# Kernel tuning notes

Measured on AMD Instinct MI355X. Metric: run time of the kernel, lower is better.

Reference implementation:

```python
import jax, jax.numpy as jnp
import numpy as np

N = 50000      # amino-acid nodes
DIN = 64       # input feature dim
DH = 64        # hidden dim (= GAT out_feats per head)
H = 4          # attention heads
E_RES, E_SEQ, E_KNN = 400000, 100000, 400000
EPS = 1e-5


def setup_inputs() -> dict:
    key = jax.random.key(0)
    ks = iter(jax.random.split(key, 32))
    def nrm(shape, scale=0.1):
        return jax.random.normal(next(ks), shape, dtype=jnp.float32) * scale
    def edges(E):
        s = jax.random.randint(next(ks), (E,), 0, N, dtype=jnp.int32)
        d = jax.random.randint(next(ks), (E,), 0, N, dtype=jnp.int32)
        return s, d
    x = nrm((N, DIN), 1.0)
    src_res, dst_res = edges(E_RES)
    src_seq, dst_seq = edges(E_SEQ)
    src_knn, dst_knn = edges(E_KNN)
    inp = dict(x=x, src_res=src_res, dst_res=dst_res, src_seq=src_seq,
               dst_seq=dst_seq, src_knn=src_knn, dst_knn=dst_knn)
    # layer 0 (in=DIN), layer 1 (in=DH): per-relation stacked GAT params
    inp.update(W0=nrm((3, DIN, H * DH)), al0=nrm((3, H, DH)), ar0=nrm((3, H, DH)),
               b0=nrm((3, H * DH)), rW0=nrm((3, DIN, H * DH)))
    inp.update(W1=nrm((3, DH, H * DH)), al1=nrm((3, H, DH)), ar1=nrm((3, H, DH)),
               b1=nrm((3, H * DH)), rW1=nrm((3, DH, H * DH)))
    inp.update(fcW0=nrm((DH, DH)), fcb0=nrm((DH,)), fcW1=nrm((DH, DH)), fcb1=nrm((DH,)))
    inp.update(g0=jnp.ones((DIN,), jnp.float32), be0=jnp.zeros((DIN,), jnp.float32),
               g1=jnp.ones((DH,), jnp.float32), be1=jnp.zeros((DH,), jnp.float32))
    return inp


def _bn(x, g, b):
    mu = jnp.mean(x, axis=0)
    var = jnp.mean((x - mu) ** 2, axis=0)
    return (x - mu) * jax.lax.rsqrt(var + EPS) * g + b


def _gat(h, src, dst, W, al, ar, bias, rW):
    # DGL GATConv (feat_drop off in eval, residual=True via res_fc Linear, bias)
    n = h.shape[0]
    fs = (h @ W).reshape(n, H, DH)                    # [N,H,D]
    el = jnp.sum(fs * al, axis=-1)                    # [N,H]
    er = jnp.sum(fs * ar, axis=-1)
    e = jax.nn.leaky_relu(el[src] + er[dst], 0.2)     # [E,H]
    m = jax.ops.segment_max(e, dst, num_segments=n)
    a = jnp.exp(e - m[dst])
    s = jax.ops.segment_sum(a, dst, num_segments=n)
    alpha = a / s[dst]                                # edge-softmax per dst/head
    rst = jax.ops.segment_sum(alpha[:, :, None] * fs[src], dst, num_segments=n)
    return rst + (h @ rW).reshape(n, H, DH) + bias.reshape(1, H, DH)


def _layer(x, edges, W, al, ar, b, rW, fcW, fcb, g, be):
    x = _bn(x, g, be)
    h = jnp.zeros((x.shape[0], H, DH), x.dtype)
    for r, (s_, d_) in enumerate(edges):              # 3 relation types, summed
        h = h + _gat(x, s_, d_, W[r], al[r], ar[r], b[r], rW[r])
    x = jnp.mean(h, axis=1)                           # mean over heads
    return jax.nn.relu(x @ fcW + fcb)


def reference(x, src_res, dst_res, src_seq, dst_seq, src_knn, dst_knn,
              W0, al0, ar0, b0, rW0, W1, al1, ar1, b1, rW1,
              fcW0, fcb0, fcW1, fcb1, g0, be0, g1, be1):
    edges = [(src_res, dst_res), (src_seq, dst_seq), (src_knn, dst_knn)]
    x = _layer(x, edges, W0, al0, ar0, b0, rW0, fcW0, fcb0, g0, be0)
    x = _layer(x, edges, W1, al1, ar1, b1, rW1, fcW1, fcb1, g1, be1)
    return x
```

## Files before the change

### kernel.cpp

```cpp
#include <hip/hip_runtime.h>
#include <math.h>

#define NN    50000
#define DD    64
#define HH    4
#define E_RES 400000
#define E_SEQ 100000
#define E_KNN 400000
#define ETOT  (E_RES+E_SEQ+E_KNN)
#define RPS   (NN + 4)
#define MBLK  ((NN+63)/64)
#define NBLK  ((NN+255)/256)
#define ZS    800
#define KTOT  864
#define CTPS  (ETOT + 32)
#define NGRP  (NN/4)
#define AGB   ((3*NGRP)/4)
#define NBUK  98
#define TBUK  (3*NBUK)
#define EPB   4096
#define PABLK ((ETOT+EPB-1)/EPB)

typedef __attribute__((ext_vector_type(8))) short short8;
typedef __attribute__((ext_vector_type(4))) float floatx4;

__device__ inline unsigned short f2bf(float f){
  union{float f; unsigned u;} v; v.f=f;
  unsigned r = v.u + 0x7FFF + ((v.u>>16)&1);
  return (unsigned short)(r>>16);
}
__device__ inline float bf2f(unsigned short u){
  union{unsigned u; float f;} v; v.u=(unsigned)u<<16; return v.f;
}


__global__ void __launch_bounds__(256)
k_bucketcnt(const int* __restrict__ d0, const int* __restrict__ d1,
            const int* __restrict__ d2, int* __restrict__ bcnt){
  __shared__ int cnt[TBUK];
  int t = threadIdx.x;
  for(int i=t;i<TBUK;i+=256) cnt[i]=0;
  __syncthreads();
  int ebase = blockIdx.x*EPB;
  #pragma unroll
  for(int j=0;j<16;j++){
    int i = ebase + j*256 + t;
    int d, r;
    if(i < E_RES){ d=d0[i]; r=0; }
    else if(i < E_RES+E_SEQ){ d=d1[i-E_RES]; r=1; }
    else if(i < ETOT){ d=d2[i-E_RES-E_SEQ]; r=2; }
    else continue;
    atomicAdd(&cnt[r*NBUK + (d>>9)], 1);
  }
  __syncthreads();
  for(int i=t;i<TBUK;i+=256){ int c=cnt[i]; if(c) atomicAdd(&bcnt[i], c); }
}

__global__ void k_bucketscan(const int* __restrict__ bcnt,
                             int* __restrict__ bbase, int* __restrict__ bcur){
  __shared__ int sh[TBUK];
  int t = threadIdx.x;
  if(t < 64){
    int carry = 0;
    for(int c=0;c<5;c++){
      int idx = c*64 + t;
      int v = (idx < TBUK) ? bcnt[idx] : 0;
      int inc = v;
      for(int off=1; off<64; off<<=1){ int n=__shfl_up(inc, off, 64); if(t>=off) inc+=n; }
      if(idx < TBUK) sh[idx] = carry + inc - v;
      carry += __shfl(inc, 63, 64);
    }
  }
  __syncthreads();
  if(t < TBUK){ bbase[t] = sh[t]; bcur[t] = sh[t]; }
  if(t == 0) bbase[TBUK] = ETOT;
}

__global__ void __launch_bounds__(256)
k_partA(const int* __restrict__ s0, const int* __restrict__ d0,
        const int* __restrict__ s1, const int* __restrict__ d1,
        const int* __restrict__ s2, const int* __restrict__ d2,
        int* __restrict__ bcur, unsigned* __restrict__ pairs){
  __shared__ int cnt[TBUK];
  __shared__ int gb[TBUK];
  int t = threadIdx.x;
  for(int i=t;i<TBUK;i+=256) cnt[i]=0;
  __syncthreads();
  int ebase = blockIdx.x*EPB;
  unsigned meta[16], pk[16];
  #pragma unroll
  for(int j=0;j<16;j++){
    int i = ebase + j*256 + t;
    int s, d, r;
    if(i < E_RES){ s=s0[i]; d=d0[i]; r=0; }
    else if(i < E_RES+E_SEQ){ int k=i-E_RES; s=s1[k]; d=d1[k]; r=1; }
    else if(i < ETOT){ int k=i-E_RES-E_SEQ; s=s2[k]; d=d2[k]; r=2; }
    else { meta[j]=0xFFFFFFFFu; continue; }
    int bk = r*NBUK + (d>>9);
    int rk = atomicAdd(&cnt[bk], 1);
    meta[j] = ((unsigned)bk<<16) | (unsigned)rk;
    pk[j]   = ((unsigned)(d&511)<<16) | (unsigned)s;
  }
  __syncthreads();
  for(int i=t;i<TBUK;i+=256){ int c=cnt[i]; gb[i] = c ? atomicAdd(&bcur[i], c) : 0; }
  __syncthreads();
  #pragma unroll
  for(int j=0;j<16;j++){
    unsigned mt = meta[j];
    if(mt != 0xFFFFFFFFu)
      pairs[gb[mt>>16] + (mt & 0xFFFFu)] = pk[j];
  }
}

__global__ void __launch_bounds__(256)
k_partB(const unsigned* __restrict__ pairs, const int* __restrict__ bbase,
        int* __restrict__ rowptr, int* __restrict__ csr){
  int bb = blockIdx.x, r = bb / NBUK, b = bb - r*NBUK;
  int dbase = b*512, dmax = min(512, NN - dbase);
  int off = (r==0)?0:(r==1)?E_RES:(E_RES+E_SEQ);
  __shared__ int hist[512];
  __shared__ int curs[513];
  int t = threadIdx.x;
  hist[t]=0; hist[256+t]=0;
  __syncthreads();
  int beg = bbase[bb], end = bbase[bb+1];
  for(int i=beg+t; i<end; i+=256) atomicAdd(&hist[pairs[i]>>16], 1);
  __syncthreads();
  if(t < 64){
    int carry = 0;
    for(int c=0;c<8;c++){
      int v = hist[c*64+t];
      int inc = v;
      for(int o2=1; o2<64; o2<<=1){ int n=__shfl_up(inc, o2, 64); if(t>=o2) inc+=n; }
      curs[c*64+t] = (beg - off) + carry + inc - v;
      carry += __shfl(inc, 63, 64);
    }
    if(t==0) curs[512] = end - off;
  }
  __syncthreads();
  int* rp = rowptr + r*RPS + dbase;
  for(int i=t; i<=dmax; i+=256) rp[i] = curs[i];
  __syncthreads();
  for(int i=beg+t; i<end; i+=256){
    unsigned p = pairs[i];
    int pos = atomicAdd(&curs[p>>16], 1);
    csr[off + pos] = (int)(p & 0xFFFFu);
  }
}

__global__ void k_bnstats(const float* __restrict__ x, float* __restrict__ stats,
                          unsigned short* __restrict__ Abf){
  __shared__ float sh[512];
  int t = threadIdx.x, col = t & 63, rg = t >> 6;
  float s=0.f, q=0.f;
  for(int row = blockIdx.x*4 + rg; row < NN; row += gridDim.x*4){
    float v = x[(size_t)row*64 + col]; s += v; q += v*v;
    Abf[(size_t)row*64 + col] = f2bf(v);
  }
  sh[t]=s; sh[256+t]=q; __syncthreads();
  if(rg==0){
    s = sh[col]+sh[64+col]+sh[128+col]+sh[192+col];
    q = sh[256+col]+sh[320+col]+sh[384+col]+sh[448+col];
    atomicAdd(&stats[col], s); atomicAdd(&stats[64+col], q);
  }
}

__global__ void __launch_bounds__(256)
k_prep3(const float* __restrict__ stats, const float* __restrict__ g,
        const float* __restrict__ be, const float* __restrict__ W,
        const float* __restrict__ al, const float* __restrict__ ar,
        const float* __restrict__ b, const float* __restrict__ rW,
        const float* __restrict__ fcW, const float* __restrict__ fcb,
        float* __restrict__ wbufF){
  __shared__ float scale[64], shift[64];
  int t = threadIdx.x;
  if(t<64){
    float mu  = stats[t]*(1.0f/NN);
    float var = stats[64+t]*(1.0f/NN) - mu*mu;
    float sc  = g[t]*rsqrtf(var + 1e-5f);
    scale[t]=sc; shift[t]=be[t]-mu*sc;
  }
  __syncthreads();
  char* wb = (char*)wbufF;
  unsigned short* Wf = (unsigned short*)wbufF;
  float* biasF = (float*)(wb + 110592);
  int bid = blockIdx.x;
  if(bid < 52){
    __shared__ float fcWs[4096];
    for(int i=t;i<4096;i+=256) fcWs[i]=fcW[i];
    __syncthreads();
    int j = bid*16 + (t>>4);
    int cg = (t&15)*4;
    float Wrow[64];
    if(j < 64){
      for(int d=0; d<64; d++){
        float w=0.f;
        for(int r=0;r<3;r++)
          #pragma unroll
          for(int h=0;h<4;h++)
            w += rW[((size_t)(r*64+j))*256 + h*64 + d];
        Wrow[d] = scale[j]*0.25f*w;
      }
    } else {
      int jj = j-64;
      int r = jj>>8, dc = jj&255, h = dc&3, c = dc>>2;
      const float* Wp = W + ((size_t)(r*64+c))*256 + h*64;
      float sc = 0.25f*scale[c];
      #pragma unroll
      for(int d=0; d<64; d++) Wrow[d] = sc*Wp[d];
    }
    #pragma unroll
    for(int cc=0; cc<4; cc++){
      int col = cg+cc;
      float acc=0.f;
      #pragma unroll
      for(int d=0; d<64; d++) acc += Wrow[d]*fcWs[d*64+col];
      Wf[(size_t)col*KTOT + j] = f2bf(acc);
    }
  } else if(bid < 58){
    int wv = (bid-52)*4 + (t>>6);
    int r = wv >> 3, cc = wv & 7, h = cc & 3, k = t & 63;
    const float* av = ((cc>=4)?ar:al) + (r*HH+h)*64;
    const float* Wk = W + ((size_t)(r*64+k))*256 + h*64;
    float w=0.f;
    for(int d2=0; d2<64; d2++) w += Wk[d2]*av[d2];
    float* WelR = (float*)(wb + 110848 + r*2080);
    WelR[cc*64 + k] = scale[k]*w;
    float bp = shift[k]*w;
    for(int off=32; off; off>>=1) bp += __shfl_down(bp, off, 64);
    if(k==0) (WelR + 512)[cc] = bp;
  } else {
    __shared__ float S[3][64];
    __shared__ float BH[64];
    if(t<192){
      int r=t>>6, d=t&63;
      float s=0.f;
      #pragma unroll
      for(int h=0;h<4;h++){
        const float* Wp = W + (size_t)(r*64)*256 + h*64 + d;
        for(int k=0;k<64;k++) s += shift[k]*Wp[(size_t)k*256];
      }
      S[r][d]=0.25f*s;
    } else {
      int d = t-192;
      float s=0.f;
      for(int k=0;k<64;k++){
        float w=0.f;
        for(int r=0;r<3;r++)
          #pragma unroll
          for(int h=0;h<4;h++)
            w += rW[((size_t)(r*64+k))*256 + h*64 + d];
        s += shift[k]*0.25f*w;
      }
      float bb=0.f;
      for(int r=0;r<3;r++)
        #pragma unroll
        for(int h=0;h<4;h++) bb += b[r*256 + h*64 + d];
      BH[d] = s + 0.25f*bb;
    }
    __syncthreads();
    if(t<192){
      int r=t>>6, col=t&63;
      float acc=0.f;
      for(int d=0;d<64;d++) acc += S[r][d]*fcW[d*64+col];
      Wf[(size_t)col*KTOT + 832 + r] = f2bf(acc);
    } else {
      int col=t-192;
      float acc=0.f;
      for(int d=0;d<64;d++) acc += BH[d]*fcW[d*64+col];
      biasF[col] = acc + fcb[col];
    }
    if(t<64){
      for(int j=835;j<KTOT;j++) Wf[(size_t)t*KTOT + j] = 0;
    }
  }
}

__global__ void __launch_bounds__(256)
k_el3(const float* __restrict__ A, const float* __restrict__ wbufF,
      float* __restrict__ EL){
  int r = blockIdx.x / NBLK;
  const char* wb = (const char*)wbufF;
  const float* Wel = (const float*)(wb + 110848 + r*2080);
  const float* biasE = Wel + 512;
  float* ELr = EL + (size_t)r*NN*8;
  __shared__ float sw[512];
  __shared__ float sb[8];
  int t = threadIdx.x;
  sw[t]=Wel[t]; sw[256+t]=Wel[256+t];
  if(t<8) sb[t]=biasE[t];
  __syncthreads();
  int n = (blockIdx.x % NBLK)*256 + t;
  if(n>=NN) return;
  float acc[8];
  #pragma unroll
  for(int c=0;c<8;c++) acc[c]=sb[c];
  const float4* Ar = (const float4*)(A + (size_t)n*64);
  #pragma unroll
  for(int kq=0;kq<16;kq++){
    float4 a = Ar[kq];
    #pragma unroll
    for(int c=0;c<8;c++){
      const float* w = sw + c*64 + kq*4;
      acc[c] += a.x*w[0] + a.y*w[1] + a.z*w[2] + a.w*w[3];
    }
  }
  ((float4*)ELr)[n*2]   = make_float4(acc[0],acc[1],acc[2],acc[3]);
  ((float4*)ELr)[n*2+1] = make_float4(acc[4],acc[5],acc[6],acc[7]);
}

__global__ void __launch_bounds__(256)
k_edgecoef3(const float* __restrict__ EL, const int* __restrict__ rowptr,
            const int* __restrict__ csr, unsigned short* __restrict__ coefT){
  int r = blockIdx.x / NBLK;
  const float* ELr = EL + (size_t)r*NN*8;
  const int* rp = rowptr + r*RPS;
  int off = (r==0)?0:(r==1)?E_RES:(E_RES+E_SEQ);
  const int* cs = csr + off;
  unsigned short* t0 = coefT + off;
  unsigned short* t1 = coefT + (size_t)CTPS + off;
  unsigned short* t2 = coefT + (size_t)2*CTPS + off;
  unsigned short* t3 = coefT + (size_t)3*CTPS + off;
  int n = (blockIdx.x % NBLK)*256 + threadIdx.x;
  if(n>=NN) return;
  int beg = rp[n], end = rp[n+1];
  if(end<=beg) return;
  const float4 er = ((const float4*)ELr)[n*2+1];
  float m0=-1e30f,m1=-1e30f,m2=-1e30f,m3=-1e30f;
  float s0=0.f,s1=0.f,s2=0.f,s3=0.f;
  for(int i=beg;i<end;i++){
    int src = cs[i];
    float4 el = ((const float4*)ELr)[src*2];
    float e0=el.x+er.x, e1=el.y+er.y, e2=el.z+er.z, e3=el.w+er.w;
    e0 = e0>0.f? e0 : 0.2f*e0;
    e1 = e1>0.f? e1 : 0.2f*e1;
    e2 = e2>0.f? e2 : 0.2f*e2;
    e3 = e3>0.f? e3 : 0.2f*e3;
    float n0=fmaxf(m0,e0); s0=s0*__expf(m0-n0)+__expf(e0-n0); m0=n0;
    float n1=fmaxf(m1,e1); s1=s1*__expf(m1-n1)+__expf(e1-n1); m1=n1;
    float n2=fmaxf(m2,e2); s2=s2*__expf(m2-n2)+__expf(e2-n2); m2=n2;
    float n3=fmaxf(m3,e3); s3=s3*__expf(m3-n3)+__expf(e3-n3); m3=n3;
  }
  float r0=1.f/s0, r1=1.f/s1, r2=1.f/s2, r3=1.f/s3;
  for(int i=beg;i<end;i++){
    int src = cs[i];
    float4 el = ((const float4*)ELr)[src*2];
    float e0=el.x+er.x, e1=el.y+er.y, e2=el.z+er.z, e3=el.w+er.w;
    e0 = e0>0.f? e0 : 0.2f*e0;
    e1 = e1>0.f? e1 : 0.2f*e1;
    e2 = e2>0.f? e2 : 0.2f*e2;
    e3 = e3>0.f? e3 : 0.2f*e3;
    t0[i] = f2bf(__expf(e0-m0)*r0);
    t1[i] = f2bf(__expf(e1-m1)*r1);
    t2[i] = f2bf(__expf(e2-m2)*r2);
    t3[i] = f2bf(__expf(e3-m3)*r3);
  }
}

__global__ void __launch_bounds__(256)
k_aggzr(const unsigned short* __restrict__ Abf, const int* __restrict__ rowptr,
        const int* __restrict__ csr, const unsigned short* __restrict__ coefT,
        unsigned short* __restrict__ Zbf){
  int w    = blockIdx.x*4 + (threadIdx.x>>6);
  int lane = threadIdx.x & 63;
  int r = w / NGRP;
  int g = w - r*NGRP;
  int n4 = g << 2;
  int m = lane & 15, kq = lane >> 4;
  int nn = m >> 2, h = m & 3;
  const int* rp = rowptr + r*RPS;
  int off = (r==0)?0:(r==1)?E_RES:(E_RES+E_SEQ);
  const int* cs = csr + off;
  const unsigned short* cT = coefT + (size_t)h*CTPS + off;
  int rpn  = rp[n4+nn];
  int rpn1 = rp[n4+nn+1];
  unsigned dg = (unsigned)(rpn1 - rpn);
  int beg = __shfl(rpn, 0, 64);
  int end = __shfl(rpn1, 15, 64);
  floatx4 acc0={0.f,0.f,0.f,0.f};
  floatx4 acc1={0.f,0.f,0.f,0.f};
  floatx4 acc2={0.f,0.f,0.f,0.f};
  floatx4 acc3={0.f,0.f,0.f,0.f};
  for(int eb = (beg & ~31); eb < end; eb += 32){
    int p0 = eb + kq*8;
    union { uint4 q; short8 v; } af;
    af.q = *(const uint4*)(cT + p0);
    int qd = p0 - rpn;
    unsigned w0 = (((unsigned)(qd+0)<dg)?0x0000FFFFu:0u) | (((unsigned)(qd+1)<dg)?0xFFFF0000u:0u);
    unsigned w1 = (((unsigned)(qd+2)<dg)?0x0000FFFFu:0u) | (((unsigned)(qd+3)<dg)?0xFFFF0000u:0u);
    unsigned w2 = (((unsigned)(qd+4)<dg)?0x0000FFFFu:0u) | (((unsigned)(qd+5)<dg)?0xFFFF0000u:0u);
    unsigned w3 = (((unsigned)(qd+6)<dg)?0x0000FFFFu:0u) | (((unsigned)(qd+7)<dg)?0xFFFF0000u:0u);
    af.q.x &= w0; af.q.y &= w1; af.q.z &= w2; af.q.w &= w3;
    const int* csp = cs + p0;
    int s0=csp[0],s1=csp[1],s2=csp[2],s3=csp[3],s4=csp[4],s5=csp[5],s6=csp[6],s7=csp[7];
    const unsigned short* q0 = Abf + ((size_t)s0<<6) + m;
    const unsigned short* q1 = Abf + ((size_t)s1<<6) + m;
    const unsigned short* q2 = Abf + ((size_t)s2<<6) + m;
    const unsigned short* q3 = Abf + ((size_t)s3<<6) + m;
    const unsigned short* q4 = Abf + ((size_t)s4<<6) + m;
    const unsigned short* q5 = Abf + ((size_t)s5<<6) + m;
    const unsigned short* q6 = Abf + ((size_t)s6<<6) + m;
    const unsigned short* q7 = Abf + ((size_t)s7<<6) + m;
    union { unsigned u[4]; short8 v; } b0,b1,b2,b3;
    b0.u[0]=(unsigned)q0[0] |((unsigned)q1[0]<<16);
    b0.u[1]=(unsigned)q2[0] |((unsigned)q3[0]<<16);
    b0.u[2]=(unsigned)q4[0] |((unsigned)q5[0]<<16);
    b0.u[3]=(unsigned)q6[0] |((unsigned)q7[0]<<16);
    b1.u[0]=(unsigned)q0[16]|((unsigned)q1[16]<<16);
    b1.u[1]=(unsigned)q2[16]|((unsigned)q3[16]<<16);
    b1.u[2]=(unsigned)q4[16]|((unsigned)q5[16]<<16);
    b1.u[3]=(unsigned)q6[16]|((unsigned)q7[16]<<16);
    b2.u[0]=(unsigned)q0[32]|((unsigned)q1[32]<<16);
    b2.u[1]=(unsigned)q2[32]|((unsigned)q3[32]<<16);
    b2.u[2]=(unsigned)q4[32]|((unsigned)q5[32]<<16);
    b2.u[3]=(unsigned)q6[32]|((unsigned)q7[32]<<16);
    b3.u[0]=(unsigned)q0[48]|((unsigned)q1[48]<<16);
    b3.u[1]=(unsigned)q2[48]|((unsigned)q3[48]<<16);
    b3.u[2]=(unsigned)q4[48]|((unsigned)q5[48]<<16);
    b3.u[3]=(unsigned)q6[48]|((unsigned)q7[48]<<16);
    acc0 = __builtin_amdgcn_mfma_f32_16x16x32_bf16(af.v, b0.v, acc0, 0,0,0);
    acc1 = __builtin_amdgcn_mfma_f32_16x16x32_bf16(af.v, b1.v, acc1, 0,0,0);
    acc2 = __builtin_amdgcn_mfma_f32_16x16x32_bf16(af.v, b2.v, acc2, 0,0,0);
    acc3 = __builtin_amdgcn_mfma_f32_16x16x32_bf16(af.v, b3.v, acc3, 0,0,0);
  }
  size_t zb = (size_t)(n4 + kq)*ZS + (size_t)r*256 + (size_t)m*4;
  ushort4 o;
  o.x=f2bf(acc0[0]); o.y=f2bf(acc0[1]); o.z=f2bf(acc0[2]); o.w=f2bf(acc0[3]);
  *(ushort4*)(Zbf + zb)       = o;
  o.x=f2bf(acc1[0]); o.y=f2bf(acc1[1]); o.z=f2bf(acc1[2]); o.w=f2bf(acc1[3]);
  *(ushort4*)(Zbf + zb + 64)  = o;
  o.x=f2bf(acc2[0]); o.y=f2bf(acc2[1]); o.z=f2bf(acc2[2]); o.w=f2bf(acc2[3]);
  *(ushort4*)(Zbf + zb + 128) = o;
  o.x=f2bf(acc3[0]); o.y=f2bf(acc3[1]); o.z=f2bf(acc3[2]); o.w=f2bf(acc3[3]);
  *(ushort4*)(Zbf + zb + 192) = o;
  int degk = __shfl((int)dg, kq<<2, 64);
  size_t fb = (size_t)(n4+kq)*ZS + 768;
  if(m==0)
    Zbf[fb + r] = degk>0 ? (unsigned short)0x3F80 : (unsigned short)0;
  if(r==0 && m>=1){
    Zbf[fb + 2 + m] = 0;
    if(m<15) Zbf[fb + 17 + m] = 0;
  }
}

__global__ void __launch_bounds__(256)
k_mfmaZ(const unsigned short* __restrict__ Abf, const unsigned short* __restrict__ Zbf,
        const float* __restrict__ wbufF, float* __restrict__ out,
        unsigned short* __restrict__ Abf2, float* __restrict__ stats, int dostats){
  __shared__ float spart[4][2][32];
  const unsigned short* Wf = (const unsigned short*)wbufF;
  const float* biasF = (const float*)((const char*)wbufF + 110592);
  int t = threadIdx.x, wv = t>>6, lane = t&63, m = lane&15, kq = lane>>4;
  int rt = blockIdx.x >> 1, ch = blockIdx.x & 1;
  int cb = ch*2;
  int row = rt*64 + wv*16 + m;
  int rc = row < NN ? row : NN-1;
  floatx4 acc0 = {0.f,0.f,0.f,0.f};
  floatx4 acc1 = {0.f,0.f,0.f,0.f};
  const unsigned short* Arow = Abf + (size_t)rc*64;
  const unsigned short* Zrow = Zbf + (size_t)rc*ZS;
  #pragma unroll
  for(int kb=0; kb<27; kb++){
    short8 a;
    if(kb<2) a = *(const short8*)(Arow + kb*32 + kq*8);
    else     a = *(const short8*)(Zrow + (kb-2)*32 + kq*8);
    int ko = kb*32 + kq*8;
    short8 b0 = *(const short8*)(Wf + (size_t)((cb+0)*16+m)*KTOT + ko);
    short8 b1 = *(const short8*)(Wf + (size_t)((cb+1)*16+m)*KTOT + ko);
    acc0 = __builtin_amdgcn_mfma_f32_16x16x32_bf16(a, b0, acc0, 0,0,0);
    acc1 = __builtin_amdgcn_mfma_f32_16x16x32_bf16(a, b1, acc1, 0,0,0);
  }
  int orow = rt*64 + wv*16 + kq*4;
  #pragma unroll
  for(int ct=0; ct<2; ct++){
    int col = (cb+ct)*16 + m;
    int lcol = ct*16 + m;
    floatx4 acc = (ct==0)?acc0:acc1;
    float bb = biasF[col];
    float sv=0.f, qv=0.f;
    #pragma unroll
    for(int ri=0; ri<4; ri++){
      int ro = orow + ri;
      if(ro < NN){
        float v = fmaxf(acc[ri] + bb, 0.f);
        out[(size_t)ro*64 + col] = v;
        if(dostats){
          Abf2[(size_t)ro*64 + col] = f2bf(v);
          sv += v; qv += v*v;
        }
      }
    }
    if(dostats){
      sv += __shfl_xor(sv, 16, 64); qv += __shfl_xor(qv, 16, 64);
      sv += __shfl_xor(sv, 32, 64); qv += __shfl_xor(qv, 32, 64);
      if(kq==0){ spart[wv][0][lcol]=sv; spart[wv][1][lcol]=qv; }
    }
  }
  if(dostats){
    __syncthreads();
    if(t<32){
      float s = spart[0][0][t]+spart[1][0][t]+spart[2][0][t]+spart[3][0][t];
      float q = spart[0][1][t]+spart[1][1][t]+spart[2][1][t]+spart[3][1][t];
      atomicAdd(&stats[ch*32+t], s); atomicAdd(&stats[64+ch*32+t], q);
    }
  }
}

extern "C" void kernel_launch(void* const* d_in, const int* in_sizes, int n_in,
                              void* d_out, int out_size, void* d_ws, size_t ws_size,
                              hipStream_t stream){
  const float* x      =(const float*)d_in[0];
  const int* src_res  =(const int*)d_in[1];
  const int* dst_res  =(const int*)d_in[2];
  const int* src_seq  =(const int*)d_in[3];
  const int* dst_seq  =(const int*)d_in[4];
  const int* src_knn  =(const int*)d_in[5];
  const int* dst_knn  =(const int*)d_in[6];
  const float* W0 =(const float*)d_in[7];
  const float* al0=(const float*)d_in[8];
  const float* ar0=(const float*)d_in[9];
  const float* b0 =(const float*)d_in[10];
  const float* rW0=(const float*)d_in[11];
  const float* W1 =(const float*)d_in[12];
  const float* al1=(const float*)d_in[13];
  const float* ar1=(const float*)d_in[14];
  const float* b1 =(const float*)d_in[15];
  const float* rW1=(const float*)d_in[16];
  const float* fcW0=(const float*)d_in[17];
  const float* fcb0=(const float*)d_in[18];
  const float* fcW1=(const float*)d_in[19];
  const float* fcb1=(const float*)d_in[20];
  const float* g0 =(const float*)d_in[21];
  const float* be0=(const float*)d_in[22];
  const float* g1 =(const float*)d_in[23];
  const float* be1=(const float*)d_in[24];

  char* ws=(char*)d_ws;
  int*   bcnt   =(int*)  (ws+0);
  int*   bbase  =(int*)  (ws+4096);
  float* stats0 =(float*)(ws+600000);
  float* stats1 =(float*)(ws+600512);
  int*   rowptr =(int*)  (ws+601024);
  int*   bcur   =(int*)  (ws+1201088);
  int*   csr    =(int*)  (ws+1801088);
  float* wbuf   =(float*)(ws+5401088);
  unsigned short* Abf  =(unsigned short*)(ws+5526528);
  unsigned short* Zbf  =(unsigned short*)(ws+11926528UL);
  unsigned* pairs =(unsigned*)(ws+11926528UL);
  float* xbuf   =(float*)(ws+91926528UL);
  float* EL     =(float*)(ws+104726528UL);
  unsigned short* coefT=(unsigned short*)(ws+109526528UL);
  unsigned short* Abf2 =(unsigned short*)(ws+123926528UL);

  hipMemsetAsync(ws, 0, 601024, stream);

  k_bucketcnt<<<PABLK,256,0,stream>>>(dst_res,dst_seq,dst_knn,bcnt);
  k_bucketscan<<<1,512,0,stream>>>(bcnt,bbase,bcur);
  k_partA<<<PABLK,256,0,stream>>>(src_res,dst_res,src_seq,dst_seq,
                                  src_knn,dst_knn,bcur,pairs);
  k_partB<<<TBUK,256,0,stream>>>(pairs,bbase,rowptr,csr);

  k_bnstats<<<256,256,0,stream>>>(x,stats0,Abf);
  k_prep3<<<59,256,0,stream>>>(stats0,g0,be0,W0,al0,ar0,b0,rW0,fcW0,fcb0,wbuf);
  k_el3<<<3*NBLK,256,0,stream>>>(x,wbuf,EL);
  k_edgecoef3<<<3*NBLK,256,0,stream>>>(EL,rowptr,csr,coefT);
  k_aggzr<<<AGB,256,0,stream>>>(Abf,rowptr,csr,coefT,Zbf);
  k_mfmaZ<<<2*MBLK,256,0,stream>>>(Abf,Zbf,wbuf,xbuf,Abf2,stats1,1);
  k_prep3<<<59,256,0,stream>>>(stats1,g1,be1,W1,al1,ar1,b1,rW1,fcW1,fcb1,wbuf);
  k_el3<<<3*NBLK,256,0,stream>>>(xbuf,wbuf,EL);
  k_edgecoef3<<<3*NBLK,256,0,stream>>>(EL,rowptr,csr,coefT);
  k_aggzr<<<AGB,256,0,stream>>>(Abf2,rowptr,csr,coefT,Zbf);
  k_mfmaZ<<<2*MBLK,256,0,stream>>>(Abf2,Zbf,wbuf,(float*)d_out,Abf2,stats0,0);
}
```

Before: 436.2 us.

## Fuse sparse aggregation and dense MFMA projection via an LDS-resident Z tile

Merges the per-relation edge aggregation kernel and the dense MFMA projection kernel into one. Each block now aggregates all three relations for 16 nodes, holds the bf16 Z rows in shared memory, and then runs the 864-wide K MFMA to produce the output. This removes the global write and re-read of the large Z intermediate and one launch per layer. In exchange, each wave processes the three relations serially and gets fewer parallel work items. The block also carries about 26 KB of LDS, which may limit occupancy.

```diff
diff --git a/kernel.cpp b/kernel.cpp
--- a/kernel.cpp
+++ b/kernel.cpp
@@ -9,17 +9,15 @@
 #define E_KNN 400000
 #define ETOT  (E_RES+E_SEQ+E_KNN)
 #define RPS   (NN + 4)
-#define MBLK  ((NN+63)/64)
 #define NBLK  ((NN+255)/256)
-#define ZS    800
 #define KTOT  864
 #define CTPS  (ETOT + 32)
-#define NGRP  (NN/4)
-#define AGB   ((3*NGRP)/4)
 #define NBUK  98
 #define TBUK  (3*NBUK)
 #define EPB   4096
 #define PABLK ((ETOT+EPB-1)/EPB)
+#define FBLK  (NN/16)
+#define LZS   808
 
 typedef __attribute__((ext_vector_type(8))) short short8;
 typedef __attribute__((ext_vector_type(4))) float floatx4;
@@ -32,7 +30,6 @@
 __device__ inline float bf2f(unsigned short u){
   union{unsigned u; float f;} v; v.u=(unsigned)u<<16; return v.f;
 }
-
 
 __global__ void __launch_bounds__(256)
 k_bucketcnt(const int* __restrict__ d0, const int* __restrict__ d1,
@@ -358,151 +355,117 @@
 }
 
 __global__ void __launch_bounds__(256)
-k_aggzr(const unsigned short* __restrict__ Abf, const int* __restrict__ rowptr,
+k_fused(const unsigned short* __restrict__ Abf, const int* __restrict__ rowptr,
         const int* __restrict__ csr, const unsigned short* __restrict__ coefT,
-        unsigned short* __restrict__ Zbf){
-  int w    = blockIdx.x*4 + (threadIdx.x>>6);
-  int lane = threadIdx.x & 63;
-  int r = w / NGRP;
-  int g = w - r*NGRP;
-  int n4 = g << 2;
-  int m = lane & 15, kq = lane >> 4;
-  int nn = m >> 2, h = m & 3;
-  const int* rp = rowptr + r*RPS;
-  int off = (r==0)?0:(r==1)?E_RES:(E_RES+E_SEQ);
-  const int* cs = csr + off;
-  const unsigned short* cT = coefT + (size_t)h*CTPS + off;
-  int rpn  = rp[n4+nn];
-  int rpn1 = rp[n4+nn+1];
-  unsigned dg = (unsigned)(rpn1 - rpn);
-  int beg = __shfl(rpn, 0, 64);
-  int end = __shfl(rpn1, 15, 64);
-  floatx4 acc0={0.f,0.f,0.f,0.f};
-  floatx4 acc1={0.f,0.f,0.f,0.f};
-  floatx4 acc2={0.f,0.f,0.f,0.f};
-  floatx4 acc3={0.f,0.f,0.f,0.f};
-  for(int eb = (beg & ~31); eb < end; eb += 32){
-    int p0 = eb + kq*8;
-    union { uint4 q; short8 v; } af;
-    af.q = *(const uint4*)(cT + p0);
-    int qd = p0 - rpn;
-    unsigned w0 = (((unsigned)(qd+0)<dg)?0x0000FFFFu:0u) | (((unsigned)(qd+1)<dg)?0xFFFF0000u:0u);
-    unsigned w1 = (((unsigned)(qd+2)<dg)?0x0000FFFFu:0u) | (((unsigned)(qd+3)<dg)?0xFFFF0000u:0u);
-    unsigned w2 = (((unsigned)(qd+4)<dg)?0x0000FFFFu:0u) | (((unsigned)(qd+5)<dg)?0xFFFF0000u:0u);
-    unsigned w3 = (((unsigned)(qd+6)<dg)?0x0000FFFFu:0u) | (((unsigned)(qd+7)<dg)?0xFFFF0000u:0u);
-    af.q.x &= w0; af.q.y &= w1; af.q.z &= w2; af.q.w &= w3;
-    const int* csp = cs + p0;
-    int s0=csp[0],s1=csp[1],s2=csp[2],s3=csp[3],s4=csp[4],s5=csp[5],s6=csp[6],s7=csp[7];
-    const unsigned short* q0 = Abf + ((size_t)s0<<6) + m;
-    const unsigned short* q1 = Abf + ((size_t)s1<<6) + m;
-    const unsigned short* q2 = Abf + ((size_t)s2<<6) + m;
-    const unsigned short* q3 = Abf + ((size_t)s3<<6) + m;
-    const unsigned short* q4 = Abf + ((size_t)s4<<6) + m;
-    const unsigned short* q5 = Abf + ((size_t)s5<<6) + m;
-    const unsigned short* q6 = Abf + ((size_t)s6<<6) + m;
-    const unsigned short* q7 = Abf + ((size_t)s7<<6) + m;
-    union { unsigned u[4]; short8 v; } b0,b1,b2,b3;
-    b0.u[0]=(unsigned)q0[0] |((unsigned)q1[0]<<16);
-    b0.u[1]=(unsigned)q2[0] |((unsigned)q3[0]<<16);
-    b0.u[2]=(unsigned)q4[0] |((unsigned)q5[0]<<16);
-    b0.u[3]=(unsigned)q6[0] |((unsigned)q7[0]<<16);
-    b1.u[0]=(unsigned)q0[16]|((unsigned)q1[16]<<16);
-    b1.u[1]=(unsigned)q2[16]|((unsigned)q3[16]<<16);
-    b1.u[2]=(unsigned)q4[16]|((unsigned)q5[16]<<16);
-    b1.u[3]=(unsigned)q6[16]|((unsigned)q7[16]<<16);
-    b2.u[0]=(unsigned)q0[32]|((unsigned)q1[32]<<16);
-    b2.u[1]=(unsigned)q2[32]|((unsigned)q3[32]<<16);
-    b2.u[2]=(unsigned)q4[32]|((unsigned)q5[32]<<16);
-    b2.u[3]=(unsigned)q6[32]|((unsigned)q7[32]<<16);
-    b3.u[0]=(unsigned)q0[48]|((unsigned)q1[48]<<16);
-    b3.u[1]=(unsigned)q2[48]|((unsigned)q3[48]<<16);
-    b3.u[2]=(unsigned)q4[48]|((unsigned)q5[48]<<16);
-    b3.u[3]=(unsigned)q6[48]|((unsigned)q7[48]<<16);
-    acc0 = __builtin_amdgcn_mfma_f32_16x16x32_bf16(af.v, b0.v, acc0, 0,0,0);
-    acc1 = __builtin_amdgcn_mfma_f32_16x16x32_bf16(af.v, b1.v, acc1, 0,0,0);
-    acc2 = __builtin_amdgcn_mfma_f32_16x16x32_bf16(af.v, b2.v, acc2, 0,0,0);
-    acc3 = __builtin_amdgcn_mfma_f32_16x16x32_bf16(af.v, b3.v, acc3, 0,0,0);
-  }
-  size_t zb = (size_t)(n4 + kq)*ZS + (size_t)r*256 + (size_t)m*4;
-  ushort4 o;
-  o.x=f2bf(acc0[0]); o.y=f2bf(acc0[1]); o.z=f2bf(acc0[2]); o.w=f2bf(acc0[3]);
-  *(ushort4*)(Zbf + zb)       = o;
-  o.x=f2bf(acc1[0]); o.y=f2bf(acc1[1]); o.z=f2bf(acc1[2]); o.w=f2bf(acc1[3]);
-  *(ushort4*)(Zbf + zb + 64)  = o;
-  o.x=f2bf(acc2[0]); o.y=f2bf(acc2[1]); o.z=f2bf(acc2[2]); o.w=f2bf(acc2[3]);
-  *(ushort4*)(Zbf + zb + 128) = o;
-  o.x=f2bf(acc3[0]); o.y=f2bf(acc3[1]); o.z=f2bf(acc3[2]); o.w=f2bf(acc3[3]);
-  *(ushort4*)(Zbf + zb + 192) = o;
-  int degk = __shfl((int)dg, kq<<2, 64);
-  size_t fb = (size_t)(n4+kq)*ZS + 768;
-  if(m==0)
-    Zbf[fb + r] = degk>0 ? (unsigned short)0x3F80 : (unsigned short)0;
-  if(r==0 && m>=1){
-    Zbf[fb + 2 + m] = 0;
-    if(m<15) Zbf[fb + 17 + m] = 0;
-  }
-}
-
-__global__ void __launch_bounds__(256)
-k_mfmaZ(const unsigned short* __restrict__ Abf, const unsigned short* __restrict__ Zbf,
         const float* __restrict__ wbufF, float* __restrict__ out,
         unsigned short* __restrict__ Abf2, float* __restrict__ stats, int dostats){
-  __shared__ float spart[4][2][32];
+  __shared__ unsigned short Zl[16*LZS];
   const unsigned short* Wf = (const unsigned short*)wbufF;
   const float* biasF = (const float*)((const char*)wbufF + 110592);
   int t = threadIdx.x, wv = t>>6, lane = t&63, m = lane&15, kq = lane>>4;
-  int rt = blockIdx.x >> 1, ch = blockIdx.x & 1;
-  int cb = ch*2;
-  int row = rt*64 + wv*16 + m;
-  int rc = row < NN ? row : NN-1;
-  floatx4 acc0 = {0.f,0.f,0.f,0.f};
-  floatx4 acc1 = {0.f,0.f,0.f,0.f};
-  const unsigned short* Arow = Abf + (size_t)rc*64;
-  const unsigned short* Zrow = Zbf + (size_t)rc*ZS;
+  int nb = blockIdx.x*16;
+  int n4 = nb + wv*4;
+  int nn = m>>2, h = m&3;
+  for(int i=t; i<512; i+=256){ int nd=i>>5, j=i&31; if(j<29) Zl[nd*LZS+771+j]=0; }
+  for(int r=0;r<3;r++){
+    const int* rp = rowptr + r*RPS;
+    int off = (r==0)?0:(r==1)?E_RES:(E_RES+E_SEQ);
+    const int* cs = csr + off;
+    const unsigned short* cT = coefT + (size_t)h*CTPS + off;
+    int rpn  = rp[n4+nn];
+    int rpn1 = rp[n4+nn+1];
+    unsigned dg = (unsigned)(rpn1 - rpn);
+    int beg = __shfl(rpn, 0, 64);
+    int end = __shfl(rpn1, 15, 64);
+    floatx4 acc0={0.f,0.f,0.f,0.f};
+    floatx4 acc1={0.f,0.f,0.f,0.f};
+    floatx4 acc2={0.f,0.f,0.f,0.f};
+    floatx4 acc3={0.f,0.f,0.f,0.f};
+    for(int eb = (beg & ~31); eb < end; eb += 32){
+      int p0 = eb + kq*8;
+      union { uint4 q; short8 v; } af;
+      af.q = *(const uint4*)(cT + p0);
+      int qd = p0 - rpn;
+      unsigned w0 = (((unsigned)(qd+0)<dg)?0x0000FFFFu:0u) | (((unsigned)(qd+1)<dg)?0xFFFF0000u:0u);
+      unsigned w1 = (((unsigned)(qd+2)<dg)?0x0000FFFFu:0u) | (((unsigned)(qd+3)<dg)?0xFFFF0000u:0u);
+      unsigned w2 = (((unsigned)(qd+4)<dg)?0x0000FFFFu:0u) | (((unsigned)(qd+5)<dg)?0xFFFF0000u:0u);
+      unsigned w3 = (((unsigned)(qd+6)<dg)?0x0000FFFFu:0u) | (((unsigned)(qd+7)<dg)?0xFFFF0000u:0u);
+      af.q.x &= w0; af.q.y &= w1; af.q.z &= w2; af.q.w &= w3;
+      const int* csp = cs + p0;
+      int s0=csp[0],s1=csp[1],s2=csp[2],s3=csp[3],s4=csp[4],s5=csp[5],s6=csp[6],s7=csp[7];
+      const unsigned short* q0 = Abf + ((size_t)s0<<6) + m;
+      const unsigned short* q1 = Abf + ((size_t)s1<<6) + m;
+      const unsigned short* q2 = Abf + ((size_t)s2<<6) + m;
+      const unsigned short* q3 = Abf + ((size_t)s3<<6) + m;
+      const unsigned short* q4 = Abf + ((size_t)s4<<6) + m;
+      const unsigned short* q5 = Abf + ((size_t)s5<<6) + m;
+      const unsigned short* q6 = Abf + ((size_t)s6<<6) + m;
+      const unsigned short* q7 = Abf + ((size_t)s7<<6) + m;
+      union { unsigned u[4]; short8 v; } b0,b1,b2,b3;
+      b0.u[0]=(unsigned)q0[0] |((unsigned)q1[0]<<16);
+      b0.u[1]=(unsigned)q2[0] |((unsigned)q3[0]<<16);
+      b0.u[2]=(unsigned)q4[0] |((unsigned)q5[0]<<16);
+      b0.u[3]=(unsigned)q6[0] |((unsigned)q7[0]<<16);
+      b1.u[0]=(unsigned)q0[16]|((unsigned)q1[16]<<16);
+      b1.u[1]=(unsigned)q2[16]|((unsigned)q3[16]<<16);
+      b1.u[2]=(unsigned)q4[16]|((unsigned)q5[16]<<16);
+      b1.u[3]=(unsigned)q6[16]|((unsigned)q7[16]<<16);
+      b2.u[0]=(unsigned)q0[32]|((unsigned)q1[32]<<16);
+      b2.u[1]=(unsigned)q2[32]|((unsigned)q3[32]<<16);
+      b2.u[2]=(unsigned)q4[32]|((unsigned)q5[32]<<16);
+      b2.u[3]=(unsigned)q6[32]|((unsigned)q7[32]<<16);
+      b3.u[0]=(unsigned)q0[48]|((unsigned)q1[48]<<16);
+      b3.u[1]=(unsigned)q2[48]|((unsigned)q3[48]<<16);
+      b3.u[2]=(unsigned)q4[48]|((unsigned)q5[48]<<16);
+      b3.u[3]=(unsigned)q6[48]|((unsigned)q7[48]<<16);
+      acc0 = __builtin_amdgcn_mfma_f32_16x16x32_bf16(af.v, b0.v, acc0, 0,0,0);
+      acc1 = __builtin_amdgcn_mfma_f32_16x16x32_bf16(af.v, b1.v, acc1, 0,0,0);
+      acc2 = __builtin_amdgcn_mfma_f32_16x16x32_bf16(af.v, b2.v, acc2, 0,0,0);
+      acc3 = __builtin_amdgcn_mfma_f32_16x16x32_bf16(af.v, b3.v, acc3, 0,0,0);
+    }
+    unsigned short* zrow = Zl + (wv*4+kq)*LZS + r*256 + m*4;
+    ushort4 o;
+    o.x=f2bf(acc0[0]); o.y=f2bf(acc0[1]); o.z=f2bf(acc0[2]); o.w=f2bf(acc0[3]);
+    *(ushort4*)(zrow)       = o;
+    o.x=f2bf(acc1[0]); o.y=f2bf(acc1[1]); o.z=f2bf(acc1[2]); o.w=f2bf(acc1[3]);
+    *(ushort4*)(zrow + 64)  = o;
+    o.x=f2bf(acc2[0]); o.y=f2bf(acc2[1]); o.z=f2bf(acc2[2]); o.w=f2bf(acc2[3]);
+    *(ushort4*)(zrow + 128) = o;
+    o.x=f2bf(acc3[0]); o.y=f2bf(acc3[1]); o.z=f2bf(acc3[2]); o.w=f2bf(acc3[3]);
+    *(ushort4*)(zrow + 192) = o;
+    int degk = __shfl((int)dg, kq<<2, 64);
+    if(m==0)
+      Zl[(wv*4+kq)*LZS + 768 + r] = degk>0 ? (unsigned short)0x3F80 : (unsigned short)0;
+  }
+  __syncthreads();
+  floatx4 acc = {0.f,0.f,0.f,0.f};
+  const unsigned short* Arow = Abf + (size_t)(nb+m)*64;
+  const unsigned short* Zrow = Zl + m*LZS;
   #pragma unroll
   for(int kb=0; kb<27; kb++){
     short8 a;
     if(kb<2) a = *(const short8*)(Arow + kb*32 + kq*8);
     else     a = *(const short8*)(Zrow + (kb-2)*32 + kq*8);
-    int ko = kb*32 + kq*8;
-    short8 b0 = *(const short8*)(Wf + (size_t)((cb+0)*16+m)*KTOT + ko);
-    short8 b1 = *(const short8*)(Wf + (size_t)((cb+1)*16+m)*KTOT + ko);
-    acc0 = __builtin_amdgcn_mfma_f32_16x16x32_bf16(a, b0, acc0, 0,0,0);
-    acc1 = __builtin_amdgcn_mfma_f32_16x16x32_bf16(a, b1, acc1, 0,0,0);
-  }
-  int orow = rt*64 + wv*16 + kq*4;
-  #pragma unroll
-  for(int ct=0; ct<2; ct++){
-    int col = (cb+ct)*16 + m;
-    int lcol = ct*16 + m;
-    floatx4 acc = (ct==0)?acc0:acc1;
-    float bb = biasF[col];
-    float sv=0.f, qv=0.f;
-    #pragma unroll
-    for(int ri=0; ri<4; ri++){
-      int ro = orow + ri;
-      if(ro < NN){
-        float v = fmaxf(acc[ri] + bb, 0.f);
-        out[(size_t)ro*64 + col] = v;
-        if(dostats){
-          Abf2[(size_t)ro*64 + col] = f2bf(v);
-          sv += v; qv += v*v;
-        }
-      }
-    }
+    short8 b = *(const short8*)(Wf + (size_t)(wv*16+m)*KTOT + kb*32 + kq*8);
+    acc = __builtin_amdgcn_mfma_f32_16x16x32_bf16(a, b, acc, 0,0,0);
+  }
+  int col = wv*16 + m;
+  float bb = biasF[col];
+  float sv=0.f, qv=0.f;
+  #pragma unroll
+  for(int ri=0; ri<4; ri++){
+    int ro = nb + kq*4 + ri;
+    float v = fmaxf(acc[ri] + bb, 0.f);
+    out[(size_t)ro*64 + col] = v;
     if(dostats){
-      sv += __shfl_xor(sv, 16, 64); qv += __shfl_xor(qv, 16, 64);
-      sv += __shfl_xor(sv, 32, 64); qv += __shfl_xor(qv, 32, 64);
-      if(kq==0){ spart[wv][0][lcol]=sv; spart[wv][1][lcol]=qv; }
+      Abf2[(size_t)ro*64 + col] = f2bf(v);
+      sv += v; qv += v*v;
     }
   }
   if(dostats){
-    __syncthreads();
-    if(t<32){
-      float s = spart[0][0][t]+spart[1][0][t]+spart[2][0][t]+spart[3][0][t];
-      float q = spart[0][1][t]+spart[1][1][t]+spart[2][1][t]+spart[3][1][t];
-      atomicAdd(&stats[ch*32+t], s); atomicAdd(&stats[64+ch*32+t], q);
-    }
+    sv += __shfl_xor(sv, 16, 64); qv += __shfl_xor(qv, 16, 64);
+    sv += __shfl_xor(sv, 32, 64); qv += __shfl_xor(qv, 32, 64);
+    if(kq==0){ atomicAdd(&stats[col], sv); atomicAdd(&stats[64+col], qv); }
   }
 }
 
@@ -545,7 +508,6 @@
   int*   csr    =(int*)  (ws+1801088);
   float* wbuf   =(float*)(ws+5401088);
   unsigned short* Abf  =(unsigned short*)(ws+5526528);
-  unsigned short* Zbf  =(unsigned short*)(ws+11926528UL);
   unsigned* pairs =(unsigned*)(ws+11926528UL);
   float* xbuf   =(float*)(ws+91926528UL);
   float* EL     =(float*)(ws+104726528UL);
@@ -564,11 +526,9 @@
   k_prep3<<<59,256,0,stream>>>(stats0,g0,be0,W0,al0,ar0,b0,rW0,fcW0,fcb0,wbuf);
   k_el3<<<3*NBLK,256,0,stream>>>(x,wbuf,EL);
   k_edgecoef3<<<3*NBLK,256,0,stream>>>(EL,rowptr,csr,coefT);
-  k_aggzr<<<AGB,256,0,stream>>>(Abf,rowptr,csr,coefT,Zbf);
-  k_mfmaZ<<<2*MBLK,256,0,stream>>>(Abf,Zbf,wbuf,xbuf,Abf2,stats1,1);
+  k_fused<<<FBLK,256,0,stream>>>(Abf,rowptr,csr,coefT,wbuf,xbuf,Abf2,stats1,1);
   k_prep3<<<59,256,0,stream>>>(stats1,g1,be1,W1,al1,ar1,b1,rW1,fcW1,fcb1,wbuf);
   k_el3<<<3*NBLK,256,0,stream>>>(xbuf,wbuf,EL);
   k_edgecoef3<<<3*NBLK,256,0,stream>>>(EL,rowptr,csr,coefT);
-  k_aggzr<<<AGB,256,0,stream>>>(Abf2,rowptr,csr,coefT,Zbf);
-  k_mfmaZ<<<2*MBLK,256,0,stream>>>(Abf2,Zbf,wbuf,(float*)d_out,Abf2,stats0,0);
-}
+  k_fused<<<FBLK,256,0,stream>>>(Abf2,rowptr,csr,coefT,wbuf,(float*)d_out,Abf2,stats0,0);
+}
```

Measured after the change: 430.5 us. Within noise of the previous version (-1.3%).
